# Optimization experiments

Measured on AMD Instinct MI355X. Metric: run time of the kernel, lower is better.

## Reference

```python
import jax, jax.numpy as jnp
import numpy as np

B, S, D, M = 2, 4096, 128, 64

def _linear_init(key, shape, fan_in):
    bound = 1.0 / np.sqrt(fan_in)
    return jax.random.uniform(key, shape, jnp.float32, -bound, bound)

def setup_inputs() -> dict:
    key = jax.random.key(0)
    ks = jax.random.split(key, 18)
    x = jax.random.normal(ks[0], (B, S, D), jnp.float32)
    context = jax.random.normal(ks[1], (B, S, D), jnp.float32)
    # per-mechanism params (torch Linear semantics: y = x @ W.T + b)
    Wt = _linear_init(ks[2], (M, D, D), D)   # transform weight, laid out [m, in, out]
    bt = _linear_init(ks[3], (M, D), D)
    char = jax.random.normal(ks[4], (M, D), jnp.float32)  # characteristics [1,1,d] per mech
    Wg = _linear_init(ks[5], (M, D), D)      # timing_gate weight (out=1)
    bg = _linear_init(ks[6], (M,), D)
    Wv = _linear_init(ks[7], (M, D), D)      # victory_detector weight (out=1)
    bv = _linear_init(ks[8], (M,), D)
    O = jax.random.normal(ks[9], (M, M), jnp.float32) * 0.02  # overcoming matrix
    # selector: Linear(2D,2D) -> GELU -> Linear(2D,M)
    W1 = _linear_init(ks[10], (2 * D, 2 * D), 2 * D)
    b1 = _linear_init(ks[11], (2 * D,), 2 * D)
    W2 = _linear_init(ks[12], (2 * D, M), 2 * D)
    b2 = _linear_init(ks[13], (M,), 2 * D)
    # integrate: Linear(2D, D)
    Wi = _linear_init(ks[14], (2 * D, D), 2 * D)
    bi = _linear_init(ks[15], (D,), 2 * D)
    return {"x": x, "context": context, "Wt": Wt, "bt": bt, "char": char,
            "Wg": Wg, "bg": bg, "Wv": Wv, "bv": bv, "O": O,
            "W1": W1, "b1": b1, "W2": W2, "b2": b2, "Wi": Wi, "bi": bi}

def reference(x, context, Wt, bt, char, Wg, bg, Wv, bv, O, W1, b1, W2, b2, Wi, bi):
    # selection scores over mechanisms
    sel_in = jnp.concatenate([x, context], axis=-1)          # [b,s,2d]
    h = jax.nn.gelu(sel_in @ W1 + b1, approximate=False)
    selection_scores = jax.nn.softmax(h @ W2 + b2, axis=-1)  # [b,s,m]
    # all 64 mechanism nodes as one batched GEMM
    transformed = jnp.einsum('bsd,mde->bsme', x, Wt) + bt + char   # [b,s,m,d]
    timing = jax.nn.sigmoid(jnp.einsum('bsd,md->bsm', x, Wg) + bg)  # [b,s,m]
    victory = jax.nn.sigmoid(jnp.einsum('bsme,me->bsm', transformed, Wv) + bv)
    outputs = transformed * timing[..., None]                # [b,s,m,d]
    # strategic overcoming modulation: gate = 1 + tanh(scores @ O)
    gates = 1.0 + jnp.tanh(selection_scores @ O)             # [b,s,m]
    selected = jnp.einsum('bsme,bsm->bse', outputs, gates * selection_scores)
    victory_potential = jnp.sum(victory * selection_scores, axis=-1)  # [b,s]
    integrated = jnp.concatenate([x, selected], axis=-1) @ Wi + bi    # [b,s,d]
    return integrated, victory_potential
```

## Files before the change

kernel.cpp:

```cpp
#include <hip/hip_runtime.h>
#include <hip/hip_bf16.h>


typedef __bf16 bf16_t;
typedef __bf16 bf16x8 __attribute__((ext_vector_type(8)));
typedef float  f32x4  __attribute__((ext_vector_type(4)));

#define WS_WTT      0u
#define WS_W1T      2097152u
#define WS_W2T      2228224u
#define WS_OT       2260992u
#define WS_WG       2269184u
#define WS_U        2285568u
#define WS_CVEC     2301952u
#define WS_BCT      2302208u
#define WS_WIT      2318592u

#define VP_OFF 1048576

__device__ __forceinline__ f32x4 mfma16(bf16x8 a, bf16x8 b, f32x4 c) {
  return __builtin_amdgcn_mfma_f32_16x16x32_bf16(a, b, c, 0, 0, 0);
}

__device__ __forceinline__ float gelu_exact(float v) {
  return 0.5f * v * (1.0f + erff(v * 0.70710678118654752f));
}
__device__ __forceinline__ float sigmoidf_(float v) {
  return 1.0f / (1.0f + __expf(-v));
}

__device__ __forceinline__ bf16x8 cvt8(float4 v0, float4 v1) {
  bf16x8 a;
  a[0] = (bf16_t)v0.x; a[1] = (bf16_t)v0.y; a[2] = (bf16_t)v0.z; a[3] = (bf16_t)v0.w;
  a[4] = (bf16_t)v1.x; a[5] = (bf16_t)v1.y; a[6] = (bf16_t)v1.z; a[7] = (bf16_t)v1.w;
  return a;
}

__global__ __launch_bounds__(256) void kprep(
    const float* __restrict__ Wt, const float* __restrict__ bt,
    const float* __restrict__ ch, const float* __restrict__ Wg,
    const float* __restrict__ Wv, const float* __restrict__ bv,
    const float* __restrict__ O, const float* __restrict__ W1,
    const float* __restrict__ W2, const float* __restrict__ Wi,
    char* __restrict__ ws)
{
  const int bid = blockIdx.x, tid = threadIdx.x;
  if (bid < 128) {
    const int m = bid >> 1, half = bid & 1;
    const float* wtm = Wt + m * 16384;
    bf16_t* wtt = (bf16_t*)(ws + WS_WTT) + m * 16384;
    const int ks = half * 2 + (tid >> 7), e = tid & 127;
    bf16_t tmp[32];
    #pragma unroll
    for (int dd = 0; dd < 32; ++dd)
      tmp[dd] = (bf16_t)wtm[(ks * 32 + dd) * 128 + e];
    bf16_t* dst = wtt + ks * 4096 + e * 32;
    #pragma unroll
    for (int g = 0; g < 4; ++g)
      *(bf16x8*)(dst + g * 8) = *(const bf16x8*)(tmp + g * 8);
  } else if (bid < 144) {
    int base = (bid - 128) * 256 + tid;
    int k = base >> 4, c0 = (base & 15) * 16;
    bf16_t* o = (bf16_t*)(ws + WS_W1T);
    #pragma unroll
    for (int j = 0; j < 16; ++j) o[(c0 + j) * 256 + k] = (bf16_t)W1[k * 256 + c0 + j];
  } else if (bid < 146) {
    int base = (bid - 144) * 256 + tid;
    int k = base >> 1, c0 = (base & 1) * 32;
    bf16_t* o = (bf16_t*)(ws + WS_W2T);
    #pragma unroll
    for (int j = 0; j < 32; ++j) o[(c0 + j) * 256 + k] = (bf16_t)W2[k * 64 + c0 + j];
  } else if (bid == 146) {
    int k = tid >> 2, c0 = (tid & 3) * 16;
    bf16_t* o = (bf16_t*)(ws + WS_OT);
    #pragma unroll
    for (int j = 0; j < 16; ++j) o[(c0 + j) * 64 + k] = (bf16_t)O[k * 64 + c0 + j];
  } else if (bid == 147) {
    bf16_t* o = (bf16_t*)(ws + WS_WG);
    #pragma unroll
    for (int j = 0; j < 32; ++j) o[tid * 32 + j] = (bf16_t)Wg[tid * 32 + j];
  } else if (bid == 148) {
    bf16_t* o = (bf16_t*)(ws + WS_BCT);
    #pragma unroll
    for (int i = 0; i < 4; ++i) {
      int task = tid + i * 256;
      int m = task >> 4, e0 = (task & 15) * 8;
      #pragma unroll
      for (int j = 0; j < 8; ++j)
        o[(e0 + j) * 64 + m] = (bf16_t)(bt[m * 128 + e0 + j] + ch[m * 128 + e0 + j]);
    }
  } else if (bid < 153) {
    int base = (bid - 149) * 256 + tid;
    int k = base >> 2, c0 = (base & 3) * 32;
    bf16_t* o = (bf16_t*)(ws + WS_WIT);
    #pragma unroll
    for (int j = 0; j < 32; ++j) o[(c0 + j) * 256 + k] = (bf16_t)Wi[k * 128 + c0 + j];
  } else if (bid < 185) {
    int task = (bid - 153) * 256 + tid;
    int m = task >> 7, d = task & 127;
    const float4* wp = (const float4*)(Wt + m * 16384 + d * 128);
    const float4* vp = (const float4*)(Wv + m * 128);
    float s = 0.f;
    #pragma unroll
    for (int i = 0; i < 32; ++i) {
      float4 a = wp[i], b = vp[i];
      s += a.x * b.x + a.y * b.y + a.z * b.z + a.w * b.w;
    }
    ((bf16_t*)(ws + WS_U))[m * 128 + d] = (bf16_t)s;
  } else {
    if (tid < 64) {
      int m = tid;
      const float4* bp = (const float4*)(bt + m * 128);
      const float4* cp = (const float4*)(ch + m * 128);
      const float4* vp = (const float4*)(Wv + m * 128);
      float s = bv[m];
      #pragma unroll
      for (int i = 0; i < 32; ++i) {
        float4 a = bp[i], c = cp[i], b = vp[i];
        s += (a.x + c.x) * b.x + (a.y + c.y) * b.y + (a.z + c.z) * b.z + (a.w + c.w) * b.w;
      }
      ((float*)(ws + WS_CVEC))[m] = s;
    }
  }
}

__device__ __forceinline__ void loadF(bf16x8 (&F)[4], const char* bbase, int m) {
  const char* p = bbase + m * 32768;
  F[0] = *(const bf16x8*)(p);
  F[1] = *(const bf16x8*)(p + 8192);
  F[2] = *(const bf16x8*)(p + 16384);
  F[3] = *(const bf16x8*)(p + 24576);
}

template<int J>
__device__ __forceinline__ void computeT(const bf16x8 (&F)[4], const f32x4 (&wc)[8],
                                         const bf16x8 (&aX)[2][4], f32x4 (&acc)[2]) {
  #pragma unroll
  for (int rg = 0; rg < 2; ++rg) {
    f32x4 y = {0.f, 0.f, 0.f, 0.f};
    #pragma unroll
    for (int ks = 0; ks < 4; ++ks) y = mfma16(aX[rg][ks], F[ks], y);
    #pragma unroll
    for (int jj = 0; jj < 4; ++jj)
      acc[rg][jj] += wc[rg * 4 + jj][J] * y[jj];
  }
}

__global__ __launch_bounds__(512, 2) void kfused(
    const float* __restrict__ x, const float* __restrict__ ctx,
    const float* __restrict__ b1, const float* __restrict__ b2,
    const float* __restrict__ bg, const float* __restrict__ bi,
    char* __restrict__ ws, float* __restrict__ out)
{
  __shared__ char sm[92160];
  bf16_t* hL      = (bf16_t*)sm;
  float*  scoresL = (float*)(sm + 32768);
  float*  wL      = (float*)(sm + 49152);
  bf16_t* scbL    = (bf16_t*)(sm + 66560);
  bf16_t* wbL     = (bf16_t*)(sm + 74752);
  bf16_t* selL    = (bf16_t*)(sm + 82944);
  float*  vpL     = (float*)(sm + 91136);

  const int tid = threadIdx.x;
  const int lane = tid & 63, wid = tid >> 6;
  const int rh = wid >> 2;
  const int wq = wid & 3;
  const int tb = (blockIdx.x >> 1) * 64;
  const int eh = blockIdx.x & 1;
  const int lr = lane & 15;
  const int lg = lane >> 4;
  const int lk = lg * 8;
  const int lj4 = lg * 4;
  const int wr = rh * 32;

  const bf16_t* W1t = (const bf16_t*)(ws + WS_W1T);
  const bf16_t* W2t = (const bf16_t*)(ws + WS_W2T);
  const bf16_t* Ot  = (const bf16_t*)(ws + WS_OT);
  const bf16_t* Wgb = (const bf16_t*)(ws + WS_WG);
  const bf16_t* Ub  = (const bf16_t*)(ws + WS_U);
  const float*  cv  = (const float*)(ws + WS_CVEC);
  const bf16_t* bct = (const bf16_t*)(ws + WS_BCT);
  const bf16_t* Wit = (const bf16_t*)(ws + WS_WIT);
  const char*  wttc = (const char*)(ws + WS_WTT);

  bf16x8 aX[2][4];
  #pragma unroll
  for (int rg = 0; rg < 2; ++rg) {
    const float* xr = x + (tb + wr + rg * 16 + lr) * 128;
    #pragma unroll
    for (int ks = 0; ks < 4; ++ks)
      aX[rg][ks] = cvt8(*(const float4*)(xr + ks * 32 + lk),
                        *(const float4*)(xr + ks * 32 + lk + 4));
  }

  {
    f32x4 a1[4][2] = {{{0,0,0,0},{0,0,0,0}},{{0,0,0,0},{0,0,0,0}},
                      {{0,0,0,0},{0,0,0,0}},{{0,0,0,0},{0,0,0,0}}};
    #pragma unroll
    for (int ks = 0; ks < 8; ++ks) {
      bf16x8 af[2];
      if (ks < 4) {
        af[0] = aX[0][ks]; af[1] = aX[1][ks];
      } else {
        #pragma unroll
        for (int rg = 0; rg < 2; ++rg) {
          const float* cr = ctx + (tb + wr + rg * 16 + lr) * 128 + (ks - 4) * 32 + lk;
          af[rg] = cvt8(*(const float4*)cr, *(const float4*)(cr + 4));
        }
      }
      #pragma unroll
      for (int cg = 0; cg < 4; ++cg) {
        bf16x8 b = *(const bf16x8*)(W1t + (wq * 64 + cg * 16 + lr) * 256 + ks * 32 + lk);
        a1[cg][0] = mfma16(af[0], b, a1[cg][0]);
        a1[cg][1] = mfma16(af[1], b, a1[cg][1]);
      }
    }
    #pragma unroll
    for (int cg = 0; cg < 4; ++cg) {
      int c = wq * 64 + cg * 16 + lr;
      float bb = b1[c];
      #pragma unroll
      for (int rg = 0; rg < 2; ++rg)
        #pragma unroll
        for (int j = 0; j < 4; ++j) {
          int r = wr + rg * 16 + lj4 + j;
          float v = gelu_exact(a1[cg][rg][j] + bb);
          *(bf16_t*)((char*)hL + ((r * 512 + c * 2) ^ ((r & 7) << 4))) = (bf16_t)v;
        }
    }
  }
  __syncthreads();

  {
    int c = wq * 16 + lr;
    f32x4 l[2] = {{0,0,0,0},{0,0,0,0}};
    #pragma unroll
    for (int ks = 0; ks < 8; ++ks) {
      int k0 = ks * 32 + lk;
      bf16x8 b = *(const bf16x8*)(W2t + c * 256 + k0);
      #pragma unroll
      for (int rg = 0; rg < 2; ++rg) {
        int r = wr + rg * 16 + lr;
        bf16x8 a = *(const bf16x8*)((char*)hL + ((r * 512 + k0 * 2) ^ ((r & 7) << 4)));
        l[rg] = mfma16(a, b, l[rg]);
      }
    }
    float bb = b2[c];
    #pragma unroll
    for (int rg = 0; rg < 2; ++rg)
      #pragma unroll
      for (int j = 0; j < 4; ++j)
        scoresL[(wr + rg * 16 + lj4 + j) * 64 + c] = l[rg][j] + bb;
  }
  __syncthreads();

  {
    int row = tid >> 3, i = tid & 7;
    float v[8];
    #pragma unroll
    for (int j = 0; j < 8; ++j) v[j] = scoresL[row * 64 + i * 8 + j];
    float mx = v[0];
    #pragma unroll
    for (int j = 1; j < 8; ++j) mx = fmaxf(mx, v[j]);
    mx = fmaxf(mx, __shfl_xor(mx, 1));
    mx = fmaxf(mx, __shfl_xor(mx, 2));
    mx = fmaxf(mx, __shfl_xor(mx, 4));
    float sum = 0.f;
    #pragma unroll
    for (int j = 0; j < 8; ++j) { v[j] = __expf(v[j] - mx); sum += v[j]; }
    sum += __shfl_xor(sum, 1);
    sum += __shfl_xor(sum, 2);
    sum += __shfl_xor(sum, 4);
    float inv = 1.0f / sum;
    #pragma unroll
    for (int j = 0; j < 8; ++j) {
      float s = v[j] * inv;
      int cc = i * 8 + j;
      scoresL[row * 64 + cc] = s;
      *(bf16_t*)((char*)scbL + ((row * 128 + cc * 2) ^ ((row & 7) << 4))) = (bf16_t)s;
    }
  }
  __syncthreads();

  {
    const int c = wq * 16 + lr;
    f32x4 g[2] = {{0,0,0,0},{0,0,0,0}};
    #pragma unroll
    for (int ks = 0; ks < 2; ++ks) {
      int k0 = ks * 32 + lk;
      bf16x8 b = *(const bf16x8*)(Ot + c * 64 + k0);
      #pragma unroll
      for (int rg = 0; rg < 2; ++rg) {
        int r = wr + rg * 16 + lr;
        bf16x8 a = *(const bf16x8*)((char*)scbL + ((r * 128 + k0 * 2) ^ ((r & 7) << 4)));
        g[rg] = mfma16(a, b, g[rg]);
      }
    }
    f32x4 t[2] = {{0,0,0,0},{0,0,0,0}};
    f32x4 v[2] = {{0,0,0,0},{0,0,0,0}};
    #pragma unroll
    for (int ks = 0; ks < 4; ++ks) {
      bf16x8 bT = *(const bf16x8*)(Wgb + c * 128 + ks * 32 + lk);
      bf16x8 bV = *(const bf16x8*)(Ub  + c * 128 + ks * 32 + lk);
      #pragma unroll
      for (int rg = 0; rg < 2; ++rg) {
        t[rg] = mfma16(aX[rg][ks], bT, t[rg]);
        v[rg] = mfma16(aX[rg][ks], bV, v[rg]);
      }
    }
    float bgc = bg[c], cvc = cv[c];
    #pragma unroll
    for (int rg = 0; rg < 2; ++rg)
      #pragma unroll
      for (int j = 0; j < 4; ++j) {
        int r = wr + rg * 16 + lj4 + j;
        float gate = 1.0f + tanhf(g[rg][j]);
        float tim  = sigmoidf_(t[rg][j] + bgc);
        float vic  = sigmoidf_(v[rg][j] + cvc);
        float sc   = scoresL[r * 64 + c];
        float w    = gate * sc * tim;
        wL[r * 68 + c] = w;
        *(bf16_t*)((char*)wbL + ((r * 128 + c * 2) ^ ((r & 7) << 4))) = (bf16_t)w;
        float pv = vic * sc;
        pv += __shfl_xor(pv, 1); pv += __shfl_xor(pv, 2);
        pv += __shfl_xor(pv, 4); pv += __shfl_xor(pv, 8);
        if (lr == 0) vpL[r * 4 + wq] = pv;
      }
  }
  __syncthreads();

  if (eh == 0 && tid < 64) {
    float s = vpL[tid * 4 + 0] + vpL[tid * 4 + 1] + vpL[tid * 4 + 2] + vpL[tid * 4 + 3];
    out[VP_OFF + tb + tid] = s;
  }

  f32x4 acc[2] = {{0,0,0,0},{0,0,0,0}};
  {
    int eg = eh * 64 + wq * 16 + lr;
    #pragma unroll
    for (int ks = 0; ks < 2; ++ks) {
      int k0 = ks * 32 + lk;
      bf16x8 b = *(const bf16x8*)(bct + eg * 64 + k0);
      #pragma unroll
      for (int rg = 0; rg < 2; ++rg) {
        int r = wr + rg * 16 + lr;
        bf16x8 a = *(const bf16x8*)((char*)wbL + ((r * 128 + k0 * 2) ^ ((r & 7) << 4)));
        acc[rg] = mfma16(a, b, acc[rg]);
      }
    }
  }

  const char* bbase = wttc + (size_t)(((eh * 64 + wq * 16 + lr) * 32 + lg * 8) * 2);
  bf16x8 F0[4], F1[4], F2[4], F3[4];
  loadF(F0, bbase, 0);
  loadF(F1, bbase, 1);
  loadF(F2, bbase, 2);

  for (int it = 0; it < 16; ++it) {
    const int base = it * 4;
    f32x4 wc[8];
    #pragma unroll
    for (int rg = 0; rg < 2; ++rg)
      #pragma unroll
      for (int jj = 0; jj < 4; ++jj)
        wc[rg * 4 + jj] = *(const f32x4*)(&wL[(wr + rg * 16 + lj4 + jj) * 68 + base]);
    int n4 = base + 4 > 63 ? 63 : base + 4;
    int n5 = base + 5 > 63 ? 63 : base + 5;
    int n6 = base + 6 > 63 ? 63 : base + 6;
    loadF(F3, bbase, base + 3);
    computeT<0>(F0, wc, aX, acc);
    loadF(F0, bbase, n4);
    computeT<1>(F1, wc, aX, acc);
    loadF(F1, bbase, n5);
    computeT<2>(F2, wc, aX, acc);
    loadF(F2, bbase, n6);
    computeT<3>(F3, wc, aX, acc);
  }

  #pragma unroll
  for (int rg = 0; rg < 2; ++rg)
    #pragma unroll
    for (int j = 0; j < 4; ++j) {
      int r = wr + rg * 16 + lj4 + j;
      int cl = wq * 16 + lr;
      *(bf16_t*)((char*)selL + ((r * 128 + cl * 2) ^ ((r & 7) << 4))) = (bf16_t)acc[rg][j];
    }
  __syncthreads();

  #pragma unroll
  for (int cg = 0; cg < 2; ++cg) {
    int c = wq * 32 + cg * 16 + lr;
    f32x4 a[2] = {{0,0,0,0},{0,0,0,0}};
    #pragma unroll
    for (int ks = 0; ks < 2; ++ks) {
      int k0 = ks * 32 + lk;
      bf16x8 b = *(const bf16x8*)(Wit + c * 256 + 128 + eh * 64 + k0);
      #pragma unroll
      for (int rg = 0; rg < 2; ++rg) {
        int r = wr + rg * 16 + lr;
        bf16x8 av = *(const bf16x8*)((char*)selL + ((r * 128 + k0 * 2) ^ ((r & 7) << 4)));
        a[rg] = mfma16(av, b, a[rg]);
      }
    }
    if (eh == 0) {
      #pragma unroll
      for (int ks = 0; ks < 4; ++ks) {
        bf16x8 b = *(const bf16x8*)(Wit + c * 256 + ks * 32 + lk);
        #pragma unroll
        for (int rg = 0; rg < 2; ++rg) a[rg] = mfma16(aX[rg][ks], b, a[rg]);
      }
    }
    float bb = (eh == 0) ? bi[c] : 0.0f;
    #pragma unroll
    for (int rg = 0; rg < 2; ++rg)
      #pragma unroll
      for (int j = 0; j < 4; ++j)
        atomicAdd(&out[(tb + wr + rg * 16 + lj4 + j) * 128 + c], a[rg][j] + bb);
  }
}

extern "C" void kernel_launch(void* const* d_in, const int* in_sizes, int n_in,
                              void* d_out, int out_size, void* d_ws, size_t ws_size,
                              hipStream_t stream)
{
  (void)in_sizes; (void)n_in; (void)ws_size;
  const float* x   = (const float*)d_in[0];
  const float* ctx = (const float*)d_in[1];
  const float* Wt  = (const float*)d_in[2];
  const float* bt  = (const float*)d_in[3];
  const float* ch  = (const float*)d_in[4];
  const float* Wg  = (const float*)d_in[5];
  const float* bg  = (const float*)d_in[6];
  const float* Wv  = (const float*)d_in[7];
  const float* bv  = (const float*)d_in[8];
  const float* O   = (const float*)d_in[9];
  const float* W1  = (const float*)d_in[10];
  const float* b1  = (const float*)d_in[11];
  const float* W2  = (const float*)d_in[12];
  const float* b2  = (const float*)d_in[13];
  const float* Wi  = (const float*)d_in[14];
  const float* bi  = (const float*)d_in[15];
  float* out = (float*)d_out;
  char* ws = (char*)d_ws;

  hipMemsetAsync(d_out, 0, (size_t)out_size * 4, stream);
  kprep<<<186, 256, 0, stream>>>(Wt, bt, ch, Wg, Wv, bv, O, W1, W2, Wi, ws);
  kfused<<<256, 512, 0, stream>>>(x, ctx, b1, b2, bg, bi, ws, out);
}
```

Before: 159.8 us.

## Halve rows per block and deepen the mechanism-weight prefetch pipeline

The fused kernel now runs 256-thread blocks, each covering 32 tokens instead of 64, and the grid doubles to 512 blocks. Shared memory per block is roughly halved, and the per-mechanism weight buffer is stored transposed so each mechanism's row weights load as contiguous vectors. The main loop over the 64 mechanisms is fully unrolled and keeps eight register buffers of Wt fragments, prefetching six mechanisms ahead instead of three, to hide global-load latency. In exchange, each block streams the same Wt half for only half as many rows, which doubles weight traffic, and register pressure rises from the larger prefetch buffers.

```diff
diff --git a/kernel.cpp b/kernel.cpp
--- a/kernel.cpp
+++ b/kernel.cpp
@@ -132,46 +132,31 @@
   F[3] = *(const bf16x8*)(p + 24576);
 }
 
-template<int J>
-__device__ __forceinline__ void computeT(const bf16x8 (&F)[4], const f32x4 (&wc)[8],
-                                         const bf16x8 (&aX)[2][4], f32x4 (&acc)[2]) {
-  #pragma unroll
-  for (int rg = 0; rg < 2; ++rg) {
-    f32x4 y = {0.f, 0.f, 0.f, 0.f};
-    #pragma unroll
-    for (int ks = 0; ks < 4; ++ks) y = mfma16(aX[rg][ks], F[ks], y);
-    #pragma unroll
-    for (int jj = 0; jj < 4; ++jj)
-      acc[rg][jj] += wc[rg * 4 + jj][J] * y[jj];
-  }
-}
-
-__global__ __launch_bounds__(512, 2) void kfused(
+#define SM_BYTES 46592
+
+__global__ __launch_bounds__(256, 2) void kfused(
     const float* __restrict__ x, const float* __restrict__ ctx,
     const float* __restrict__ b1, const float* __restrict__ b2,
     const float* __restrict__ bg, const float* __restrict__ bi,
     char* __restrict__ ws, float* __restrict__ out)
 {
-  __shared__ char sm[92160];
+  __shared__ char sm[SM_BYTES];
   bf16_t* hL      = (bf16_t*)sm;
-  float*  scoresL = (float*)(sm + 32768);
-  float*  wL      = (float*)(sm + 49152);
-  bf16_t* scbL    = (bf16_t*)(sm + 66560);
-  bf16_t* wbL     = (bf16_t*)(sm + 74752);
-  bf16_t* selL    = (bf16_t*)(sm + 82944);
-  float*  vpL     = (float*)(sm + 91136);
+  float*  scoresL = (float*)(sm + 16384);
+  float*  wLT     = (float*)(sm + 24576);
+  bf16_t* scbL    = (bf16_t*)(sm + 33792);
+  bf16_t* wbL     = (bf16_t*)(sm + 37888);
+  bf16_t* selL    = (bf16_t*)(sm + 41984);
+  float*  vpL     = (float*)(sm + 46080);
 
   const int tid = threadIdx.x;
-  const int lane = tid & 63, wid = tid >> 6;
-  const int rh = wid >> 2;
-  const int wq = wid & 3;
-  const int tb = (blockIdx.x >> 1) * 64;
+  const int lane = tid & 63, wq = tid >> 6;
+  const int tb = (blockIdx.x >> 1) * 32;
   const int eh = blockIdx.x & 1;
   const int lr = lane & 15;
   const int lg = lane >> 4;
   const int lk = lg * 8;
   const int lj4 = lg * 4;
-  const int wr = rh * 32;
 
   const bf16_t* W1t = (const bf16_t*)(ws + WS_W1T);
   const bf16_t* W2t = (const bf16_t*)(ws + WS_W2T);
@@ -186,7 +171,7 @@
   bf16x8 aX[2][4];
   #pragma unroll
   for (int rg = 0; rg < 2; ++rg) {
-    const float* xr = x + (tb + wr + rg * 16 + lr) * 128;
+    const float* xr = x + (tb + rg * 16 + lr) * 128;
     #pragma unroll
     for (int ks = 0; ks < 4; ++ks)
       aX[rg][ks] = cvt8(*(const float4*)(xr + ks * 32 + lk),
@@ -204,7 +189,7 @@
       } else {
         #pragma unroll
         for (int rg = 0; rg < 2; ++rg) {
-          const float* cr = ctx + (tb + wr + rg * 16 + lr) * 128 + (ks - 4) * 32 + lk;
+          const float* cr = ctx + (tb + rg * 16 + lr) * 128 + (ks - 4) * 32 + lk;
           af[rg] = cvt8(*(const float4*)cr, *(const float4*)(cr + 4));
         }
       }
@@ -223,7 +208,7 @@
       for (int rg = 0; rg < 2; ++rg)
         #pragma unroll
         for (int j = 0; j < 4; ++j) {
-          int r = wr + rg * 16 + lj4 + j;
+          int r = rg * 16 + lj4 + j;
           float v = gelu_exact(a1[cg][rg][j] + bb);
           *(bf16_t*)((char*)hL + ((r * 512 + c * 2) ^ ((r & 7) << 4))) = (bf16_t)v;
         }
@@ -240,7 +225,7 @@
       bf16x8 b = *(const bf16x8*)(W2t + c * 256 + k0);
       #pragma unroll
       for (int rg = 0; rg < 2; ++rg) {
-        int r = wr + rg * 16 + lr;
+        int r = rg * 16 + lr;
         bf16x8 a = *(const bf16x8*)((char*)hL + ((r * 512 + k0 * 2) ^ ((r & 7) << 4)));
         l[rg] = mfma16(a, b, l[rg]);
       }
@@ -250,7 +235,7 @@
     for (int rg = 0; rg < 2; ++rg)
       #pragma unroll
       for (int j = 0; j < 4; ++j)
-        scoresL[(wr + rg * 16 + lj4 + j) * 64 + c] = l[rg][j] + bb;
+        scoresL[(rg * 16 + lj4 + j) * 64 + c] = l[rg][j] + bb;
   }
   __syncthreads();
 
@@ -291,7 +276,7 @@
       bf16x8 b = *(const bf16x8*)(Ot + c * 64 + k0);
       #pragma unroll
       for (int rg = 0; rg < 2; ++rg) {
-        int r = wr + rg * 16 + lr;
+        int r = rg * 16 + lr;
         bf16x8 a = *(const bf16x8*)((char*)scbL + ((r * 128 + k0 * 2) ^ ((r & 7) << 4)));
         g[rg] = mfma16(a, b, g[rg]);
       }
@@ -313,13 +298,13 @@
     for (int rg = 0; rg < 2; ++rg)
       #pragma unroll
       for (int j = 0; j < 4; ++j) {
-        int r = wr + rg * 16 + lj4 + j;
+        int r = rg * 16 + lj4 + j;
         float gate = 1.0f + tanhf(g[rg][j]);
         float tim  = sigmoidf_(t[rg][j] + bgc);
         float vic  = sigmoidf_(v[rg][j] + cvc);
         float sc   = scoresL[r * 64 + c];
         float w    = gate * sc * tim;
-        wL[r * 68 + c] = w;
+        wLT[c * 36 + r] = w;
         *(bf16_t*)((char*)wbL + ((r * 128 + c * 2) ^ ((r & 7) << 4))) = (bf16_t)w;
         float pv = vic * sc;
         pv += __shfl_xor(pv, 1); pv += __shfl_xor(pv, 2);
@@ -329,7 +314,7 @@
   }
   __syncthreads();
 
-  if (eh == 0 && tid < 64) {
+  if (eh == 0 && tid < 32) {
     float s = vpL[tid * 4 + 0] + vpL[tid * 4 + 1] + vpL[tid * 4 + 2] + vpL[tid * 4 + 3];
     out[VP_OFF + tb + tid] = s;
   }
@@ -343,7 +328,7 @@
       bf16x8 b = *(const bf16x8*)(bct + eg * 64 + k0);
       #pragma unroll
       for (int rg = 0; rg < 2; ++rg) {
-        int r = wr + rg * 16 + lr;
+        int r = rg * 16 + lr;
         bf16x8 a = *(const bf16x8*)((char*)wbL + ((r * 128 + k0 * 2) ^ ((r & 7) << 4)));
         acc[rg] = mfma16(a, b, acc[rg]);
       }
@@ -351,37 +336,43 @@
   }
 
   const char* bbase = wttc + (size_t)(((eh * 64 + wq * 16 + lr) * 32 + lg * 8) * 2);
-  bf16x8 F0[4], F1[4], F2[4], F3[4];
-  loadF(F0, bbase, 0);
-  loadF(F1, bbase, 1);
-  loadF(F2, bbase, 2);
-
-  for (int it = 0; it < 16; ++it) {
-    const int base = it * 4;
-    f32x4 wc[8];
-    #pragma unroll
-    for (int rg = 0; rg < 2; ++rg)
-      #pragma unroll
-      for (int jj = 0; jj < 4; ++jj)
-        wc[rg * 4 + jj] = *(const f32x4*)(&wL[(wr + rg * 16 + lj4 + jj) * 68 + base]);
-    int n4 = base + 4 > 63 ? 63 : base + 4;
-    int n5 = base + 5 > 63 ? 63 : base + 5;
-    int n6 = base + 6 > 63 ? 63 : base + 6;
-    loadF(F3, bbase, base + 3);
-    computeT<0>(F0, wc, aX, acc);
-    loadF(F0, bbase, n4);
-    computeT<1>(F1, wc, aX, acc);
-    loadF(F1, bbase, n5);
-    computeT<2>(F2, wc, aX, acc);
-    loadF(F2, bbase, n6);
-    computeT<3>(F3, wc, aX, acc);
+  bf16x8 F[8][4];
+  loadF(F[0], bbase, 0);
+  loadF(F[1], bbase, 1);
+  loadF(F[2], bbase, 2);
+  loadF(F[3], bbase, 3);
+  loadF(F[4], bbase, 4);
+  loadF(F[5], bbase, 5);
+
+  #pragma unroll
+  for (int it = 0; it < 8; ++it) {
+    const int base = it * 8;
+    #pragma unroll
+    for (int s = 0; s < 8; ++s) {
+      const int m = base + s;
+      int mp = m + 6; if (mp > 63) mp = 63;
+      loadF(F[(s + 6) & 7], bbase, mp);
+      f32x4 w0 = *(const f32x4*)(&wLT[m * 36 + lj4]);
+      f32x4 w1 = *(const f32x4*)(&wLT[m * 36 + 16 + lj4]);
+      f32x4 y0 = {0.f,0.f,0.f,0.f}, y1 = {0.f,0.f,0.f,0.f};
+      #pragma unroll
+      for (int ks = 0; ks < 4; ++ks) {
+        y0 = mfma16(aX[0][ks], F[s][ks], y0);
+        y1 = mfma16(aX[1][ks], F[s][ks], y1);
+      }
+      #pragma unroll
+      for (int jj = 0; jj < 4; ++jj) {
+        acc[0][jj] += w0[jj] * y0[jj];
+        acc[1][jj] += w1[jj] * y1[jj];
+      }
+    }
   }
 
   #pragma unroll
   for (int rg = 0; rg < 2; ++rg)
     #pragma unroll
     for (int j = 0; j < 4; ++j) {
-      int r = wr + rg * 16 + lj4 + j;
+      int r = rg * 16 + lj4 + j;
       int cl = wq * 16 + lr;
       *(bf16_t*)((char*)selL + ((r * 128 + cl * 2) ^ ((r & 7) << 4))) = (bf16_t)acc[rg][j];
     }
@@ -397,7 +388,7 @@
       bf16x8 b = *(const bf16x8*)(Wit + c * 256 + 128 + eh * 64 + k0);
       #pragma unroll
       for (int rg = 0; rg < 2; ++rg) {
-        int r = wr + rg * 16 + lr;
+        int r = rg * 16 + lr;
         bf16x8 av = *(const bf16x8*)((char*)selL + ((r * 128 + k0 * 2) ^ ((r & 7) << 4)));
         a[rg] = mfma16(av, b, a[rg]);
       }
@@ -415,7 +406,7 @@
     for (int rg = 0; rg < 2; ++rg)
       #pragma unroll
       for (int j = 0; j < 4; ++j)
-        atomicAdd(&out[(tb + wr + rg * 16 + lj4 + j) * 128 + c], a[rg][j] + bb);
+        atomicAdd(&out[(tb + rg * 16 + lj4 + j) * 128 + c], a[rg][j] + bb);
   }
 }
 
@@ -445,5 +436,5 @@
 
   hipMemsetAsync(d_out, 0, (size_t)out_size * 4, stream);
   kprep<<<186, 256, 0, stream>>>(Wt, bt, ch, Wg, Wv, bv, O, W1, W2, Wi, ws);
-  kfused<<<256, 512, 0, stream>>>(x, ctx, b1, b2, bg, bi, ws, out);
-}
+  kfused<<<512, 256, 0, stream>>>(x, ctx, b1, b2, bg, bi, ws, out);
+}
```

New measurement: 156.3 us. -2.2%, faster.
